# Optimization experiments

Hardware: AMD Instinct MI355X
Metric: run time of the kernel (lower is better)

Reference implementation:

```python
import jax, jax.numpy as jnp
import numpy as np
from jax import lax

K = 3          # kernel_size
STRIDE = 1
PAD = 1
DIL = 1


def conv2d(x, w, b):
    y = lax.conv_general_dilated(
        x, w, (STRIDE, STRIDE), [(PAD, PAD), (PAD, PAD)],
        rhs_dilation=(DIL, DIL),
        dimension_numbers=('NCHW', 'OIHW', 'NCHW'))
    return y + b[None, :, None, None]


def setup_inputs() -> dict:
    key = jax.random.key(0)
    ks = jax.random.split(key, 6)
    N, Cin, Cout, H, W = 4, 64, 64, 192, 192
    K2 = K * K
    x_input = jax.random.normal(ks[0], (N, Cin, H, W), jnp.float32)
    # offset branch: 2*K2 output channels (dy, dx per kernel tap); small init
    w_off = jax.random.normal(ks[1], (2 * K2, Cin, K, K), jnp.float32) * 0.01
    b_off = jnp.zeros((2 * K2,), jnp.float32)
    # modulation branch (DCNv2): K2 channels, 2*sigmoid
    w_mod = jax.random.normal(ks[2], (K2, Cin, K, K), jnp.float32) * 0.01
    b_mod = jnp.zeros((K2,), jnp.float32)
    # main conv weight + bias
    w = jax.random.normal(ks[3], (Cout, Cin, K, K), jnp.float32) / np.sqrt(Cin * K2)
    b = jax.random.normal(ks[4], (Cout,), jnp.float32) * 0.01
    return {'x_input': x_input, 'w_off': w_off, 'b_off': b_off,
            'w_mod': w_mod, 'b_mod': b_mod, 'w': w, 'b': b}


def _deform_sample(x, py, px):
    # x [N,C,H,W]; py,px [N,K2,Ho,Wo] -> bilinear samples [N,C,K2,Ho,Wo]
    N, C, H, W = x.shape
    xf = x.reshape(N, C, H * W)
    y0 = jnp.floor(py)
    x0 = jnp.floor(px)
    ly = py - y0
    lx = px - x0
    y0i = y0.astype(jnp.int32)
    x0i = x0.astype(jnp.int32)

    def gather(yi, xi, wt):
        valid = (yi >= 0) & (yi < H) & (xi >= 0) & (xi < W)  # zero padding outside
        idx = jnp.clip(yi, 0, H - 1) * W + jnp.clip(xi, 0, W - 1)
        idx_flat = idx.reshape(N, -1)
        vals = jax.vmap(lambda a, i: jnp.take(a, i, axis=1))(xf, idx_flat)  # [N,C,K2*Ho*Wo]
        vals = vals.reshape(N, C, *yi.shape[1:])
        return vals * (wt * valid)[:, None]

    out = gather(y0i, x0i, (1 - ly) * (1 - lx))
    out = out + gather(y0i, x0i + 1, (1 - ly) * lx)
    out = out + gather(y0i + 1, x0i, ly * (1 - lx))
    out = out + gather(y0i + 1, x0i + 1, ly * lx)
    return out


def reference(x_input, w_off, b_off, w_mod, b_mod, w, b):
    N, C, H, W = x_input.shape
    K2 = K * K
    off = conv2d(x_input, w_off, b_off)                       # [N,2*K2,Ho,Wo]
    mod = 2.0 * jax.nn.sigmoid(conv2d(x_input, w_mod, b_mod))  # [N,K2,Ho,Wo]
    Ho, Wo = off.shape[2], off.shape[3]
    off = off.reshape(N, K2, 2, Ho, Wo)
    ky = jnp.repeat(jnp.arange(K) * DIL, K).astype(jnp.float32)  # [K2]
    kx = jnp.tile(jnp.arange(K) * DIL, K).astype(jnp.float32)
    hy = (jnp.arange(Ho) * STRIDE - PAD).astype(jnp.float32)
    wx = (jnp.arange(Wo) * STRIDE - PAD).astype(jnp.float32)
    py = off[:, :, 0] + hy[None, None, :, None] + ky[None, :, None, None]  # [N,K2,Ho,Wo]
    px = off[:, :, 1] + wx[None, None, None, :] + kx[None, :, None, None]
    val = _deform_sample(x_input, py, px) * mod[:, None]       # [N,C,K2,Ho,Wo]
    out = jnp.einsum('nckhw,ock->nohw', val, w.reshape(w.shape[0], C, K2))
    out = out + b[None, :, None, None]
    return jax.nn.relu(out)
```

## Files before the change

kernel.cpp:

```cpp
#include <hip/hip_runtime.h>
#include <hip/hip_bf16.h>
#include <hip/hip_fp16.h>
#include <math.h>


#define NB   4
#define CIN  64
#define COUT 64
#define HH   192
#define WW   192
#define HW   (HH*WW)

typedef __attribute__((ext_vector_type(4))) float f32x4;
typedef __attribute__((ext_vector_type(8))) _Float16 f16x8;
typedef __attribute__((ext_vector_type(4))) unsigned int u32x4;

__device__ __forceinline__ int iclamp(int v, int lo, int hi) {
    return v < lo ? lo : (v > hi ? hi : v);
}
__device__ __forceinline__ unsigned short f16bits(float f) {
    __half h = __float2half(f);
    union { __half h; unsigned short u; } t; t.h = h; return t.u;
}
__device__ __forceinline__ float h2f(unsigned short u) {
    union { unsigned short u; __half h; } t; t.u = u; return __half2float(t.h);
}
__device__ __forceinline__ __half2 dup_lo(unsigned int u) {
    unsigned int lo = u & 0xffffu;
    unsigned int d = lo | (lo << 16);
    union { unsigned int u; __half2 h; } t; t.u = d; return t.h;
}
__device__ __forceinline__ __half2 dup_hi(unsigned int u) {
    unsigned int hi = u >> 16;
    unsigned int d = hi | (hi << 16);
    union { unsigned int u; __half2 h; } t; t.u = d; return t.h;
}

__global__ __launch_bounds__(256) void prep_weights(
        const float* __restrict__ w, const float* __restrict__ w_off,
        const float* __restrict__ w_mod, const float* __restrict__ b_off,
        const float* __restrict__ b_mod, unsigned short* __restrict__ wfrag,
        unsigned short* __restrict__ wauxf, float* __restrict__ baux) {
    int idx = blockIdx.x * 256 + threadIdx.x;
    if (idx < 36864) {
        int j    = idx & 7;
        int lane = (idx >> 3) & 63;
        int kc   = (idx >> 9) & 1;
        int g    = (idx >> 10) & 3;
        int k    = idx >> 12;
        int o = g * 16 + (lane & 15);
        int c = kc * 32 + (lane >> 4) * 8 + j;
        wfrag[idx] = f16bits(w[(o * 64 + c) * 9 + k]);
    }
    if (idx < 18432) {
        int j    = idx & 7;
        int lane = (idx >> 3) & 63;
        int kc   = (idx >> 9) & 1;
        int ga   = (idx >> 10) & 1;
        int k    = idx >> 11;
        int o = ga * 16 + (lane & 15);
        int c = kc * 32 + (lane >> 4) * 8 + j;
        float v = 0.f;
        if (o < 18)      v = w_off[(o * 64 + c) * 9 + k];
        else if (o < 27) v = w_mod[((o - 18) * 64 + c) * 9 + k];
        wauxf[idx] = f16bits(v);
    }
    if (idx < 32) {
        float v = 0.f;
        if (idx < 18)      v = b_off[idx];
        else if (idx < 27) v = b_mod[idx - 18];
        baux[idx] = v;
    }
}

__global__ __launch_bounds__(256, 4) void dcn_fused(
        const float* __restrict__ x,
        const unsigned short* __restrict__ wfrag,
        const unsigned short* __restrict__ wauxf,
        const float* __restrict__ baux,
        const float* __restrict__ bias,
        float* __restrict__ out) {
    __shared__ __align__(16) unsigned short win[216 * 64];
    __shared__ __align__(16) unsigned short oml[2][32][32];
    __shared__ __align__(16) u32x4 plan[576];

    int tid = threadIdx.x;
    int l   = tid & 63;
    int wv  = __builtin_amdgcn_readfirstlane(tid >> 6);
    int r2  = wv >> 1;
    int g2  = wv & 1;

    int id = blockIdx.x;
    int sw = (id & 7) * 288 + (id >> 3);
    int n  = sw / 576;
    int r  = sw % 576;
    int ho2    = (r / 6) * 2;
    int wobase = (r % 6) * 32;

    const float* xn = x + (size_t)n * CIN * HW;

    if (tid < 216) {
        int rw = tid / 36, cl = tid - rw * 36;
        int gy = iclamp(ho2 - 2 + rw, 0, HH - 1);
        int gx = iclamp(wobase - 2 + cl, 0, WW - 1);
        const float* xp = xn + gy * WW + gx;
        char* dst = (char*)win + tid * 128;
        int xw = (tid & 7) << 4;
#pragma unroll
        for (int c8 = 0; c8 < 8; c8++) {
            union { unsigned short us[8]; u32x4 q; } pk8;
#pragma unroll
            for (int j = 0; j < 8; j++)
                pk8.us[j] = f16bits(xp[(c8 * 8 + j) * HW]);
            *(u32x4*)(dst + ((c8 * 16) ^ xw)) = pk8.q;
        }
    }
    __syncthreads();

    {
        f32x4 aacc[2];
        aacc[0] = (f32x4){0.f, 0.f, 0.f, 0.f};
        aacc[1] = (f32x4){0.f, 0.f, 0.f, 0.f};
        const f16x8 zero8 = (f16x8){0, 0, 0, 0, 0, 0, 0, 0};
        int pa   = g2 * 16 + (l & 15);
        int cba  = (l >> 4) * 16;
        int ho_a = ho2 + r2;

#pragma unroll 1
        for (int k = 0; k < 9; k++) {
            int ky = k / 3, kx = k - 3 * (k / 3);
            int ys = ho_a + ky - 1;
            if ((unsigned)ys >= (unsigned)HH) continue;
            int xs = wobase + pa + kx - 1;
            bool ok = (unsigned)xs < (unsigned)WW;
            int sA = (ky + 1 + r2) * 36 + (pa + kx + 1);
            const char* pp = (const char*)win + sA * 128;
            int xw = (sA & 7) << 4;
            const f16x8* wa = ((const f16x8*)wauxf) + (k * 4) * 64 + l;
#pragma unroll
            for (int kc = 0; kc < 2; kc++) {
                f16x8 bv = *(const f16x8*)(pp + ((kc * 64 + cba) ^ xw));
                if (!ok) bv = zero8;
                f16x8 a0 = wa[(kc)     * 64];
                f16x8 a1 = wa[(2 + kc) * 64];
                aacc[0] = __builtin_amdgcn_mfma_f32_16x16x32_f16(a0, bv, aacc[0], 0, 0, 0);
                aacc[1] = __builtin_amdgcn_mfma_f32_16x16x32_f16(a1, bv, aacc[1], 0, 0, 0);
            }
        }
#pragma unroll
        for (int h = 0; h < 2; h++) {
#pragma unroll
            for (int rr = 0; rr < 2; rr++) {
                int o = h * 16 + (l >> 4) * 4 + rr * 2;
                float v0 = aacc[h][rr * 2]     + baux[o];
                float v1 = aacc[h][rr * 2 + 1] + baux[o + 1];
                if (o     >= 18) v0 = 2.f / (1.f + expf(-v0));
                if (o + 1 >= 18) v1 = 2.f / (1.f + expf(-v1));
                unsigned int pk = (unsigned int)f16bits(v0)
                                | ((unsigned int)f16bits(v1) << 16);
                *(unsigned int*)&oml[r2][pa][o] = pk;
            }
        }
    }
    __syncthreads();

    for (int i = tid; i < 576; i += 256) {
        int rp = i / 9;
        int k  = i - rp * 9;
        int r2p = rp >> 5, px = rp & 31;
        int ho_p  = ho2 + r2p;
        int wox_p = wobase + px;

        int ky = k / 3, kx = k - 3 * (k / 3);
        unsigned int oyx = *(const unsigned int*)&oml[r2p][px][2 * k];
        float offy = h2f((unsigned short)(oyx & 0xffffu));
        float offx = h2f((unsigned short)(oyx >> 16));
        float mm   = h2f(oml[r2p][px][18 + k]);
        float py  = offy + (float)(ho_p - 1 + ky);
        float pxf = offx + (float)(wox_p - 1 + kx);
        float y0f = floorf(py), x0f = floorf(pxf);
        float ly = py - y0f, lx = pxf - x0f;
        int y0 = (int)y0f, x0 = (int)x0f;
        int y1 = y0 + 1, x1 = x0 + 1;
        bool y0ok = (unsigned)y0 < (unsigned)HH, y1ok = (unsigned)y1 < (unsigned)HH;
        bool x0ok = (unsigned)x0 < (unsigned)WW, x1ok = (unsigned)x1 < (unsigned)WW;
        float wt0 = (y0ok && x0ok) ? mm * (1.f - ly) * (1.f - lx) : 0.f;
        float wt1 = (y0ok && x1ok) ? mm * (1.f - ly) * lx         : 0.f;
        float wt2 = (y1ok && x0ok) ? mm * ly * (1.f - lx)         : 0.f;
        float wt3 = (y1ok && x1ok) ? mm * ly * lx                 : 0.f;
        int y0c = iclamp(y0, 0, HH - 1), y1c = iclamp(y1, 0, HH - 1);
        int x0c = iclamp(x0, 0, WW - 1), x1c = iclamp(x1, 0, WW - 1);
        int sy0 = y0c - ho2 + 2,    sy1 = y1c - ho2 + 2;
        int sx0 = x0c - wobase + 2, sx1 = x1c - wobase + 2;
        int sy0c = iclamp(sy0, 0, 5),  sy1c = iclamp(sy1, 0, 5);
        int sx0c = iclamp(sx0, 0, 35), sx1c = iclamp(sx1, 0, 35);
        bool fb0 = (wt0 > 0.f) && ((sy0 != sy0c) | (sx0 != sx0c));
        bool fb1 = (wt1 > 0.f) && ((sy0 != sy0c) | (sx1 != sx1c));
        bool fb2 = (wt2 > 0.f) && ((sy1 != sy1c) | (sx0 != sx0c));
        bool fb3 = (wt3 > 0.f) && ((sy1 != sy1c) | (sx1 != sx1c));
        unsigned int c0 = fb0 ? 0xffffu : (unsigned int)(sy0c * 36 + sx0c);
        unsigned int c1 = fb1 ? 0xffffu : (unsigned int)(sy0c * 36 + sx1c);
        unsigned int c2 = fb2 ? 0xffffu : (unsigned int)(sy1c * 36 + sx0c);
        unsigned int c3 = fb3 ? 0xffffu : (unsigned int)(sy1c * 36 + sx1c);

        unsigned int w01 = (unsigned int)f16bits(wt0) | ((unsigned int)f16bits(wt1) << 16);
        unsigned int w23 = (unsigned int)f16bits(wt2) | ((unsigned int)f16bits(wt3) << 16);
        plan[i] = (u32x4){w01, w23, c0 | (c1 << 16), c2 | (c3 << 16)};
    }
    __syncthreads();

    f32x4 acc[4];
#pragma unroll
    for (int nf = 0; nf < 4; nf++) acc[nf] = (f32x4){0.f, 0.f, 0.f, 0.f};

    int p_loc = l & 15;
    int chunk = l >> 4;
    int p     = g2 * 16 + p_loc;
    int ho_w  = ho2 + r2;
    int wox   = wobase + p;
    int cb0   = chunk * 16;
    int cb1   = cb0 + 64;
    int chb   = chunk * 8;
    const u32x4* plp = plan + (r2 * 32 + p) * 9;
    const unsigned short* omp = &oml[r2][p][0];

    union Q { u32x4 u; __half2 h2[4]; unsigned short us[8]; };

#pragma unroll 1
    for (int k = 0; k < 9; k++) {
        const f16x8* wfk = ((const f16x8*)wfrag) + (k * 8) * 64 + l;
        f16x8 wB[8];
#pragma unroll
        for (int f = 0; f < 8; f++) wB[f] = wfk[f * 64];

        u32x4 pl = plp[k];
        unsigned int c0 = pl.z & 0xffffu, c1 = pl.z >> 16;
        unsigned int c2 = pl.w & 0xffffu, c3 = pl.w >> 16;

        int d0 = (int)(c0 & 255u), d1 = (int)(c1 & 255u);
        int d2 = (int)(c2 & 255u), d3 = (int)(c3 & 255u);
        const char* b0 = (const char*)win + d0 * 128;
        const char* b1 = (const char*)win + d1 * 128;
        const char* b2 = (const char*)win + d2 * 128;
        const char* b3 = (const char*)win + d3 * 128;
        int x0 = (d0 & 7) << 4, x1 = (d1 & 7) << 4;
        int x2 = (d2 & 7) << 4, x3 = (d3 & 7) << 4;
        Q q0, q1, q2, q3, q4, q5, q6, q7;
        q0.u = *(const u32x4*)(b0 + (cb0 ^ x0));
        q1.u = *(const u32x4*)(b0 + (cb1 ^ x0));
        q2.u = *(const u32x4*)(b1 + (cb0 ^ x1));
        q3.u = *(const u32x4*)(b1 + (cb1 ^ x1));
        q4.u = *(const u32x4*)(b2 + (cb0 ^ x2));
        q5.u = *(const u32x4*)(b2 + (cb1 ^ x2));
        q6.u = *(const u32x4*)(b3 + (cb0 ^ x3));
        q7.u = *(const u32x4*)(b3 + (cb1 ^ x3));

        if (__builtin_expect((c0 == 0xffffu) | (c1 == 0xffffu) |
                             (c2 == 0xffffu) | (c3 == 0xffffu), 0)) {
            int ky = k / 3, kx = k - 3 * (k / 3);
            unsigned int oyx = *(const unsigned int*)(omp + 2 * k);
            float offy = h2f((unsigned short)(oyx & 0xffffu));
            float offx = h2f((unsigned short)(oyx >> 16));
            float py  = offy + (float)(ho_w - 1 + ky);
            float pxf = offx + (float)(wox - 1 + kx);
            int y0 = (int)floorf(py), x0i = (int)floorf(pxf);
            int y0c = iclamp(y0, 0, HH - 1),  y1c = iclamp(y0 + 1, 0, HH - 1);
            int x0c = iclamp(x0i, 0, WW - 1), x1c = iclamp(x0i + 1, 0, WW - 1);
            if (c0 == 0xffffu) {
                const float* gp = xn + y0c * WW + x0c;
#pragma unroll
                for (int j = 0; j < 8; j++) {
                    q0.us[j] = f16bits(gp[(chb + j) * HW]);
                    q1.us[j] = f16bits(gp[(chb + 32 + j) * HW]);
                }
            }
            if (c1 == 0xffffu) {
                const float* gp = xn + y0c * WW + x1c;
#pragma unroll
                for (int j = 0; j < 8; j++) {
                    q2.us[j] = f16bits(gp[(chb + j) * HW]);
                    q3.us[j] = f16bits(gp[(chb + 32 + j) * HW]);
                }
            }
            if (c2 == 0xffffu) {
                const float* gp = xn + y1c * WW + x0c;
#pragma unroll
                for (int j = 0; j < 8; j++) {
                    q4.us[j] = f16bits(gp[(chb + j) * HW]);
                    q5.us[j] = f16bits(gp[(chb + 32 + j) * HW]);
                }
            }
            if (c3 == 0xffffu) {
                const float* gp = xn + y1c * WW + x1c;
#pragma unroll
                for (int j = 0; j < 8; j++) {
                    q6.us[j] = f16bits(gp[(chb + j) * HW]);
                    q7.us[j] = f16bits(gp[(chb + 32 + j) * HW]);
                }
            }
        }

        __half2 wv0 = dup_lo(pl.x), wv1 = dup_hi(pl.x);
        __half2 wv2 = dup_lo(pl.y), wv3 = dup_hi(pl.y);
        union { __half2 h2[4]; f16x8 v; } fA0, fA1;
#pragma unroll
        for (int j = 0; j < 4; j++) {
            __half2 t = __hmul2(q0.h2[j], wv0);
            t = __hfma2(q2.h2[j], wv1, t);
            t = __hfma2(q4.h2[j], wv2, t);
            t = __hfma2(q6.h2[j], wv3, t);
            fA0.h2[j] = t;
            __half2 s = __hmul2(q1.h2[j], wv0);
            s = __hfma2(q3.h2[j], wv1, s);
            s = __hfma2(q5.h2[j], wv2, s);
            s = __hfma2(q7.h2[j], wv3, s);
            fA1.h2[j] = s;
        }

        __builtin_amdgcn_s_setprio(1);
#pragma unroll
        for (int nf = 0; nf < 4; nf++) {
            acc[nf] = __builtin_amdgcn_mfma_f32_16x16x32_f16(fA0.v, wB[nf * 2],     acc[nf], 0, 0, 0);
            acc[nf] = __builtin_amdgcn_mfma_f32_16x16x32_f16(fA1.v, wB[nf * 2 + 1], acc[nf], 0, 0, 0);
        }
        __builtin_amdgcn_s_setprio(0);
    }

#pragma unroll
    for (int nf = 0; nf < 4; nf++) {
        int o = nf * 16 + p_loc;
        float bo = bias[o];
        int wo = wobase + g2 * 16 + chunk * 4;
        float* op = out + (((size_t)n * COUT + o) * HH + ho_w) * WW + wo;
#pragma unroll
        for (int rr = 0; rr < 4; rr++) {
            float v = acc[nf][rr] + bo;
            op[rr] = fmaxf(v, 0.f);
        }
    }
}

extern "C" void kernel_launch(void* const* d_in, const int* in_sizes, int n_in,
                              void* d_out, int out_size, void* d_ws, size_t ws_size,
                              hipStream_t stream) {
    const float* x     = (const float*)d_in[0];
    const float* w_off = (const float*)d_in[1];
    const float* b_off = (const float*)d_in[2];
    const float* w_mod = (const float*)d_in[3];
    const float* b_mod = (const float*)d_in[4];
    const float* w     = (const float*)d_in[5];
    const float* b     = (const float*)d_in[6];
    float* out = (float*)d_out;

    unsigned short* wfrag = (unsigned short*)d_ws;
    unsigned short* wauxf = wfrag + 36864;
    float* baux = (float*)(wauxf + 18432);

    prep_weights<<<dim3(144), dim3(256), 0, stream>>>(w, w_off, w_mod, b_off,
                                                      b_mod, wfrag, wauxf, baux);
    dcn_fused<<<dim3(2304), dim3(256), 0, stream>>>(x, wfrag, wauxf, baux, b, out);
}
```

Before: 62.56 us.

## Split K-taps across two wave groups with LDS reduction, 512-thread blocks

New measurement: 218.8 us. +249.8%, slower.

```diff
diff --git a/kernel.cpp b/kernel.cpp
--- a/kernel.cpp
+++ b/kernel.cpp
@@ -73,7 +73,7 @@
     }
 }
 
-__global__ __launch_bounds__(256, 4) void dcn_fused(
+__global__ __launch_bounds__(512, 8) void dcn_fused(
         const float* __restrict__ x,
         const unsigned short* __restrict__ wfrag,
         const unsigned short* __restrict__ wauxf,
@@ -87,7 +87,8 @@
     int tid = threadIdx.x;
     int l   = tid & 63;
     int wv  = __builtin_amdgcn_readfirstlane(tid >> 6);
-    int r2  = wv >> 1;
+    int kh  = wv >> 2;
+    int r2  = (wv >> 1) & 1;
     int g2  = wv & 1;
 
     int id = blockIdx.x;
@@ -99,20 +100,21 @@
 
     const float* xn = x + (size_t)n * CIN * HW;
 
-    if (tid < 216) {
-        int rw = tid / 36, cl = tid - rw * 36;
-        int gy = iclamp(ho2 - 2 + rw, 0, HH - 1);
-        int gx = iclamp(wobase - 2 + cl, 0, WW - 1);
-        const float* xp = xn + gy * WW + gx;
-        char* dst = (char*)win + tid * 128;
-        int xw = (tid & 7) << 4;
-#pragma unroll
-        for (int c8 = 0; c8 < 8; c8++) {
+#pragma unroll
+    for (int pass = 0; pass < 4; pass++) {
+        int idx = pass * 512 + tid;
+        if (idx < 1728) {
+            int part = idx / 216;
+            int slot = idx - part * 216;
+            int rw = slot / 36, cl = slot - rw * 36;
+            int gy = iclamp(ho2 - 2 + rw, 0, HH - 1);
+            int gx = iclamp(wobase - 2 + cl, 0, WW - 1);
+            const float* xp = xn + gy * WW + gx;
             union { unsigned short us[8]; u32x4 q; } pk8;
 #pragma unroll
             for (int j = 0; j < 8; j++)
-                pk8.us[j] = f16bits(xp[(c8 * 8 + j) * HW]);
-            *(u32x4*)(dst + ((c8 * 16) ^ xw)) = pk8.q;
+                pk8.us[j] = f16bits(xp[(part * 8 + j) * HW]);
+            *(u32x4*)((char*)win + slot * 128 + ((part * 16) ^ ((slot & 7) << 4))) = pk8.q;
         }
     }
     __syncthreads();
@@ -137,34 +139,49 @@
             const char* pp = (const char*)win + sA * 128;
             int xw = (sA & 7) << 4;
             const f16x8* wa = ((const f16x8*)wauxf) + (k * 4) * 64 + l;
-#pragma unroll
-            for (int kc = 0; kc < 2; kc++) {
-                f16x8 bv = *(const f16x8*)(pp + ((kc * 64 + cba) ^ xw));
-                if (!ok) bv = zero8;
-                f16x8 a0 = wa[(kc)     * 64];
-                f16x8 a1 = wa[(2 + kc) * 64];
-                aacc[0] = __builtin_amdgcn_mfma_f32_16x16x32_f16(a0, bv, aacc[0], 0, 0, 0);
-                aacc[1] = __builtin_amdgcn_mfma_f32_16x16x32_f16(a1, bv, aacc[1], 0, 0, 0);
-            }
-        }
-#pragma unroll
-        for (int h = 0; h < 2; h++) {
-#pragma unroll
-            for (int rr = 0; rr < 2; rr++) {
-                int o = h * 16 + (l >> 4) * 4 + rr * 2;
-                float v0 = aacc[h][rr * 2]     + baux[o];
-                float v1 = aacc[h][rr * 2 + 1] + baux[o + 1];
-                if (o     >= 18) v0 = 2.f / (1.f + expf(-v0));
-                if (o + 1 >= 18) v1 = 2.f / (1.f + expf(-v1));
-                unsigned int pk = (unsigned int)f16bits(v0)
-                                | ((unsigned int)f16bits(v1) << 16);
-                *(unsigned int*)&oml[r2][pa][o] = pk;
+            f16x8 bv = *(const f16x8*)(pp + ((kh * 64 + cba) ^ xw));
+            if (!ok) bv = zero8;
+            f16x8 a0 = wa[(kh)     * 64];
+            f16x8 a1 = wa[(2 + kh) * 64];
+            aacc[0] = __builtin_amdgcn_mfma_f32_16x16x32_f16(a0, bv, aacc[0], 0, 0, 0);
+            aacc[1] = __builtin_amdgcn_mfma_f32_16x16x32_f16(a1, bv, aacc[1], 0, 0, 0);
+        }
+        __syncthreads();
+        float* redA = (float*)plan;
+        int ridx = (((wv & 3) * 64) + l) * 8;
+        if (kh == 1) {
+#pragma unroll
+            for (int h = 0; h < 2; h++)
+#pragma unroll
+                for (int rr = 0; rr < 4; rr++)
+                    redA[ridx + h * 4 + rr] = aacc[h][rr];
+        }
+        __syncthreads();
+        if (kh == 0) {
+#pragma unroll
+            for (int h = 0; h < 2; h++)
+#pragma unroll
+                for (int rr = 0; rr < 4; rr++)
+                    aacc[h][rr] += redA[ridx + h * 4 + rr];
+#pragma unroll
+            for (int h = 0; h < 2; h++) {
+#pragma unroll
+                for (int rr = 0; rr < 2; rr++) {
+                    int o = h * 16 + (l >> 4) * 4 + rr * 2;
+                    float v0 = aacc[h][rr * 2]     + baux[o];
+                    float v1 = aacc[h][rr * 2 + 1] + baux[o + 1];
+                    if (o     >= 18) v0 = 2.f / (1.f + expf(-v0));
+                    if (o + 1 >= 18) v1 = 2.f / (1.f + expf(-v1));
+                    unsigned int pk = (unsigned int)f16bits(v0)
+                                    | ((unsigned int)f16bits(v1) << 16);
+                    *(unsigned int*)&oml[r2][pa][o] = pk;
+                }
             }
         }
     }
     __syncthreads();
 
-    for (int i = tid; i < 576; i += 256) {
+    for (int i = tid; i < 576; i += 512) {
         int rp = i / 9;
         int k  = i - rp * 9;
         int r2p = rp >> 5, px = rp & 31;
@@ -226,8 +243,10 @@
 
     union Q { u32x4 u; __half2 h2[4]; unsigned short us[8]; };
 
+    int kbeg = kh * 5;
+    int kend = kh ? 9 : 5;
 #pragma unroll 1
-    for (int k = 0; k < 9; k++) {
+    for (int k = kbeg; k < kend; k++) {
         const f16x8* wfk = ((const f16x8*)wfrag) + (k * 8) * 64 + l;
         f16x8 wB[8];
 #pragma unroll
@@ -326,16 +345,41 @@
         __builtin_amdgcn_s_setprio(0);
     }
 
-#pragma unroll
-    for (int nf = 0; nf < 4; nf++) {
-        int o = nf * 16 + p_loc;
-        float bo = bias[o];
-        int wo = wobase + g2 * 16 + chunk * 4;
-        float* op = out + (((size_t)n * COUT + o) * HH + ho_w) * WW + wo;
-#pragma unroll
-        for (int rr = 0; rr < 4; rr++) {
-            float v = acc[nf][rr] + bo;
-            op[rr] = fmaxf(v, 0.f);
+    __syncthreads();
+    unsigned int* redM = (unsigned int*)plan;
+    if (kh == 1) {
+        int base = (tid - 256) * 8;
+#pragma unroll
+        for (int nf = 0; nf < 4; nf++)
+#pragma unroll
+            for (int rp = 0; rp < 2; rp++) {
+                unsigned int u = (unsigned int)f16bits(acc[nf][rp * 2])
+                               | ((unsigned int)f16bits(acc[nf][rp * 2 + 1]) << 16);
+                redM[base + nf * 2 + rp] = u;
+            }
+    }
+    __syncthreads();
+    if (kh == 0) {
+        int base = tid * 8;
+#pragma unroll
+        for (int nf = 0; nf < 4; nf++)
+#pragma unroll
+            for (int rp = 0; rp < 2; rp++) {
+                unsigned int u = redM[base + nf * 2 + rp];
+                acc[nf][rp * 2]     += h2f((unsigned short)(u & 0xffffu));
+                acc[nf][rp * 2 + 1] += h2f((unsigned short)(u >> 16));
+            }
+#pragma unroll
+        for (int nf = 0; nf < 4; nf++) {
+            int o = nf * 16 + p_loc;
+            float bo = bias[o];
+            int wo = wobase + g2 * 16 + chunk * 4;
+            float* op = out + (((size_t)n * COUT + o) * HH + ho_w) * WW + wo;
+#pragma unroll
+            for (int rr = 0; rr < 4; rr++) {
+                float v = acc[nf][rr] + bo;
+                op[rr] = fmaxf(v, 0.f);
+            }
         }
     }
 }
@@ -358,5 +402,5 @@
 
     prep_weights<<<dim3(144), dim3(256), 0, stream>>>(w, w_off, w_mod, b_off,
                                                       b_mod, wfrag, wauxf, baux);
-    dcn_fused<<<dim3(2304), dim3(256), 0, stream>>>(x, wfrag, wauxf, baux, b, out);
-}
+    dcn_fused<<<dim3(2304), dim3(512), 0, stream>>>(x, wfrag, wauxf, baux, b, out);
+}
```

## Compute bilinear sampling plan inline per lane instead of shared-memory plan table

Applied to the files above, without the earlier changes.

New measurement: 80.44 us. +28.6%, slower.

```diff
diff --git a/kernel.cpp b/kernel.cpp
--- a/kernel.cpp
+++ b/kernel.cpp
@@ -24,16 +24,6 @@
 }
 __device__ __forceinline__ float h2f(unsigned short u) {
     union { unsigned short u; __half h; } t; t.u = u; return __half2float(t.h);
-}
-__device__ __forceinline__ __half2 dup_lo(unsigned int u) {
-    unsigned int lo = u & 0xffffu;
-    unsigned int d = lo | (lo << 16);
-    union { unsigned int u; __half2 h; } t; t.u = d; return t.h;
-}
-__device__ __forceinline__ __half2 dup_hi(unsigned int u) {
-    unsigned int hi = u >> 16;
-    unsigned int d = hi | (hi << 16);
-    union { unsigned int u; __half2 h; } t; t.u = d; return t.h;
 }
 
 __global__ __launch_bounds__(256) void prep_weights(
@@ -73,7 +63,7 @@
     }
 }
 
-__global__ __launch_bounds__(256, 4) void dcn_fused(
+__global__ __launch_bounds__(256, 5) void dcn_fused(
         const float* __restrict__ x,
         const unsigned short* __restrict__ wfrag,
         const unsigned short* __restrict__ wauxf,
@@ -82,7 +72,6 @@
         float* __restrict__ out) {
     __shared__ __align__(16) unsigned short win[216 * 64];
     __shared__ __align__(16) unsigned short oml[2][32][32];
-    __shared__ __align__(16) u32x4 plan[576];
 
     int tid = threadIdx.x;
     int l   = tid & 63;
@@ -164,51 +153,6 @@
     }
     __syncthreads();
 
-    for (int i = tid; i < 576; i += 256) {
-        int rp = i / 9;
-        int k  = i - rp * 9;
-        int r2p = rp >> 5, px = rp & 31;
-        int ho_p  = ho2 + r2p;
-        int wox_p = wobase + px;
-
-        int ky = k / 3, kx = k - 3 * (k / 3);
-        unsigned int oyx = *(const unsigned int*)&oml[r2p][px][2 * k];
-        float offy = h2f((unsigned short)(oyx & 0xffffu));
-        float offx = h2f((unsigned short)(oyx >> 16));
-        float mm   = h2f(oml[r2p][px][18 + k]);
-        float py  = offy + (float)(ho_p - 1 + ky);
-        float pxf = offx + (float)(wox_p - 1 + kx);
-        float y0f = floorf(py), x0f = floorf(pxf);
-        float ly = py - y0f, lx = pxf - x0f;
-        int y0 = (int)y0f, x0 = (int)x0f;
-        int y1 = y0 + 1, x1 = x0 + 1;
-        bool y0ok = (unsigned)y0 < (unsigned)HH, y1ok = (unsigned)y1 < (unsigned)HH;
-        bool x0ok = (unsigned)x0 < (unsigned)WW, x1ok = (unsigned)x1 < (unsigned)WW;
-        float wt0 = (y0ok && x0ok) ? mm * (1.f - ly) * (1.f - lx) : 0.f;
-        float wt1 = (y0ok && x1ok) ? mm * (1.f - ly) * lx         : 0.f;
-        float wt2 = (y1ok && x0ok) ? mm * ly * (1.f - lx)         : 0.f;
-        float wt3 = (y1ok && x1ok) ? mm * ly * lx                 : 0.f;
-        int y0c = iclamp(y0, 0, HH - 1), y1c = iclamp(y1, 0, HH - 1);
-        int x0c = iclamp(x0, 0, WW - 1), x1c = iclamp(x1, 0, WW - 1);
-        int sy0 = y0c - ho2 + 2,    sy1 = y1c - ho2 + 2;
-        int sx0 = x0c - wobase + 2, sx1 = x1c - wobase + 2;
-        int sy0c = iclamp(sy0, 0, 5),  sy1c = iclamp(sy1, 0, 5);
-        int sx0c = iclamp(sx0, 0, 35), sx1c = iclamp(sx1, 0, 35);
-        bool fb0 = (wt0 > 0.f) && ((sy0 != sy0c) | (sx0 != sx0c));
-        bool fb1 = (wt1 > 0.f) && ((sy0 != sy0c) | (sx1 != sx1c));
-        bool fb2 = (wt2 > 0.f) && ((sy1 != sy1c) | (sx0 != sx0c));
-        bool fb3 = (wt3 > 0.f) && ((sy1 != sy1c) | (sx1 != sx1c));
-        unsigned int c0 = fb0 ? 0xffffu : (unsigned int)(sy0c * 36 + sx0c);
-        unsigned int c1 = fb1 ? 0xffffu : (unsigned int)(sy0c * 36 + sx1c);
-        unsigned int c2 = fb2 ? 0xffffu : (unsigned int)(sy1c * 36 + sx0c);
-        unsigned int c3 = fb3 ? 0xffffu : (unsigned int)(sy1c * 36 + sx1c);
-
-        unsigned int w01 = (unsigned int)f16bits(wt0) | ((unsigned int)f16bits(wt1) << 16);
-        unsigned int w23 = (unsigned int)f16bits(wt2) | ((unsigned int)f16bits(wt3) << 16);
-        plan[i] = (u32x4){w01, w23, c0 | (c1 << 16), c2 | (c3 << 16)};
-    }
-    __syncthreads();
-
     f32x4 acc[4];
 #pragma unroll
     for (int nf = 0; nf < 4; nf++) acc[nf] = (f32x4){0.f, 0.f, 0.f, 0.f};
@@ -221,8 +165,13 @@
     int cb0   = chunk * 16;
     int cb1   = cb0 + 64;
     int chb   = chunk * 8;
-    const u32x4* plp = plan + (r2 * 32 + p) * 9;
-    const unsigned short* omp = &oml[r2][p][0];
+
+    union { u32x4 q[4]; unsigned short us[32]; } om;
+    {
+        const u32x4* omp4 = (const u32x4*)&oml[r2][p][0];
+        om.q[0] = omp4[0]; om.q[1] = omp4[1];
+        om.q[2] = omp4[2]; om.q[3] = omp4[3];
+    }
 
     union Q { u32x4 u; __half2 h2[4]; unsigned short us[8]; };
 
@@ -233,40 +182,54 @@
 #pragma unroll
         for (int f = 0; f < 8; f++) wB[f] = wfk[f * 64];
 
-        u32x4 pl = plp[k];
-        unsigned int c0 = pl.z & 0xffffu, c1 = pl.z >> 16;
-        unsigned int c2 = pl.w & 0xffffu, c3 = pl.w >> 16;
-
-        int d0 = (int)(c0 & 255u), d1 = (int)(c1 & 255u);
-        int d2 = (int)(c2 & 255u), d3 = (int)(c3 & 255u);
-        const char* b0 = (const char*)win + d0 * 128;
-        const char* b1 = (const char*)win + d1 * 128;
-        const char* b2 = (const char*)win + d2 * 128;
-        const char* b3 = (const char*)win + d3 * 128;
-        int x0 = (d0 & 7) << 4, x1 = (d1 & 7) << 4;
-        int x2 = (d2 & 7) << 4, x3 = (d3 & 7) << 4;
+        int ky = k / 3, kx = k - 3 * (k / 3);
+        float offy = h2f(om.us[2 * k]);
+        float offx = h2f(om.us[2 * k + 1]);
+        float mm   = h2f(om.us[18 + k]);
+        float py  = offy + (float)(ho_w - 1 + ky);
+        float pxf = offx + (float)(wox - 1 + kx);
+        float y0f = floorf(py), x0f = floorf(pxf);
+        float ly = py - y0f, lx = pxf - x0f;
+        int y0 = (int)y0f, x0i = (int)x0f;
+        int y1 = y0 + 1, x1i = x0i + 1;
+        bool y0ok = (unsigned)y0 < (unsigned)HH, y1ok = (unsigned)y1 < (unsigned)HH;
+        bool x0ok = (unsigned)x0i < (unsigned)WW, x1ok = (unsigned)x1i < (unsigned)WW;
+        float wt0 = (y0ok && x0ok) ? mm * (1.f - ly) * (1.f - lx) : 0.f;
+        float wt1 = (y0ok && x1ok) ? mm * (1.f - ly) * lx         : 0.f;
+        float wt2 = (y1ok && x0ok) ? mm * ly * (1.f - lx)         : 0.f;
+        float wt3 = (y1ok && x1ok) ? mm * ly * lx                 : 0.f;
+        int y0c = iclamp(y0, 0, HH - 1),  y1c = iclamp(y1, 0, HH - 1);
+        int x0c = iclamp(x0i, 0, WW - 1), x1c = iclamp(x1i, 0, WW - 1);
+
+        int sy0 = y0c - ho2 + 2,    sy1 = y1c - ho2 + 2;
+        int sx0 = x0c - wobase + 2, sx1 = x1c - wobase + 2;
+        int sy0c = iclamp(sy0, 0, 5),  sy1c = iclamp(sy1, 0, 5);
+        int sx0c = iclamp(sx0, 0, 35), sx1c = iclamp(sx1, 0, 35);
+        bool fb00 = (wt0 > 0.f) && ((sy0 != sy0c) | (sx0 != sx0c));
+        bool fb01 = (wt1 > 0.f) && ((sy0 != sy0c) | (sx1 != sx1c));
+        bool fb10 = (wt2 > 0.f) && ((sy1 != sy1c) | (sx0 != sx0c));
+        bool fb11 = (wt3 > 0.f) && ((sy1 != sy1c) | (sx1 != sx1c));
+
+        int s00 = sy0c * 36 + sx0c, s01 = sy0c * 36 + sx1c;
+        int s10 = sy1c * 36 + sx0c, s11 = sy1c * 36 + sx1c;
+        const char* b0 = (const char*)win + s00 * 128;
+        const char* b1 = (const char*)win + s01 * 128;
+        const char* b2 = (const char*)win + s10 * 128;
+        const char* b3 = (const char*)win + s11 * 128;
+        int x00 = (s00 & 7) << 4, x01 = (s01 & 7) << 4;
+        int x10 = (s10 & 7) << 4, x11 = (s11 & 7) << 4;
         Q q0, q1, q2, q3, q4, q5, q6, q7;
-        q0.u = *(const u32x4*)(b0 + (cb0 ^ x0));
-        q1.u = *(const u32x4*)(b0 + (cb1 ^ x0));
-        q2.u = *(const u32x4*)(b1 + (cb0 ^ x1));
-        q3.u = *(const u32x4*)(b1 + (cb1 ^ x1));
-        q4.u = *(const u32x4*)(b2 + (cb0 ^ x2));
-        q5.u = *(const u32x4*)(b2 + (cb1 ^ x2));
-        q6.u = *(const u32x4*)(b3 + (cb0 ^ x3));
-        q7.u = *(const u32x4*)(b3 + (cb1 ^ x3));
-
-        if (__builtin_expect((c0 == 0xffffu) | (c1 == 0xffffu) |
-                             (c2 == 0xffffu) | (c3 == 0xffffu), 0)) {
-            int ky = k / 3, kx = k - 3 * (k / 3);
-            unsigned int oyx = *(const unsigned int*)(omp + 2 * k);
-            float offy = h2f((unsigned short)(oyx & 0xffffu));
-            float offx = h2f((unsigned short)(oyx >> 16));
-            float py  = offy + (float)(ho_w - 1 + ky);
-            float pxf = offx + (float)(wox - 1 + kx);
-            int y0 = (int)floorf(py), x0i = (int)floorf(pxf);
-            int y0c = iclamp(y0, 0, HH - 1),  y1c = iclamp(y0 + 1, 0, HH - 1);
-            int x0c = iclamp(x0i, 0, WW - 1), x1c = iclamp(x0i + 1, 0, WW - 1);
-            if (c0 == 0xffffu) {
+        q0.u = *(const u32x4*)(b0 + (cb0 ^ x00));
+        q1.u = *(const u32x4*)(b0 + (cb1 ^ x00));
+        q2.u = *(const u32x4*)(b1 + (cb0 ^ x01));
+        q3.u = *(const u32x4*)(b1 + (cb1 ^ x01));
+        q4.u = *(const u32x4*)(b2 + (cb0 ^ x10));
+        q5.u = *(const u32x4*)(b2 + (cb1 ^ x10));
+        q6.u = *(const u32x4*)(b3 + (cb0 ^ x11));
+        q7.u = *(const u32x4*)(b3 + (cb1 ^ x11));
+
+        if (__builtin_expect(fb00 | fb01 | fb10 | fb11, 0)) {
+            if (fb00) {
                 const float* gp = xn + y0c * WW + x0c;
 #pragma unroll
                 for (int j = 0; j < 8; j++) {
@@ -274,7 +237,7 @@
                     q1.us[j] = f16bits(gp[(chb + 32 + j) * HW]);
                 }
             }
-            if (c1 == 0xffffu) {
+            if (fb01) {
                 const float* gp = xn + y0c * WW + x1c;
 #pragma unroll
                 for (int j = 0; j < 8; j++) {
@@ -282,7 +245,7 @@
                     q3.us[j] = f16bits(gp[(chb + 32 + j) * HW]);
                 }
             }
-            if (c2 == 0xffffu) {
+            if (fb10) {
                 const float* gp = xn + y1c * WW + x0c;
 #pragma unroll
                 for (int j = 0; j < 8; j++) {
@@ -290,7 +253,7 @@
                     q5.us[j] = f16bits(gp[(chb + 32 + j) * HW]);
                 }
             }
-            if (c3 == 0xffffu) {
+            if (fb11) {
                 const float* gp = xn + y1c * WW + x1c;
 #pragma unroll
                 for (int j = 0; j < 8; j++) {
@@ -300,8 +263,10 @@
             }
         }
 
-        __half2 wv0 = dup_lo(pl.x), wv1 = dup_hi(pl.x);
-        __half2 wv2 = dup_lo(pl.y), wv3 = dup_hi(pl.y);
+        __half2 wv0 = __float2half2_rn(wt0);
+        __half2 wv1 = __float2half2_rn(wt1);
+        __half2 wv2 = __float2half2_rn(wt2);
+        __half2 wv3 = __float2half2_rn(wt3);
         union { __half2 h2[4]; f16x8 v; } fA0, fA1;
 #pragma unroll
         for (int j = 0; j < 4; j++) {
```
